# Kernel optimization log

Measured on AMD Instinct MI355X. Metric: run time of the kernel, lower is better.

The kernel has to match this reference:

```python
import jax, jax.numpy as jnp
import numpy as np

VOCAB, EMB, HID, OUT = 10, 32, 64, 10
B, T = 4096, 128

def setup_inputs() -> dict:
    key = jax.random.key(0)
    ks = jax.random.split(key, 8)
    num1 = jax.random.randint(ks[0], (B, T), 0, VOCAB, dtype=jnp.int32)
    num2 = jax.random.randint(ks[1], (B, T), 0, VOCAB, dtype=jnp.int32)
    # Glorot-ish scaled params (values irrelevant for correctness baseline)
    E = jax.random.normal(ks[2], (VOCAB, EMB), jnp.float32) * 0.05
    Wxh = jax.random.normal(ks[3], (2 * EMB, HID), jnp.float32) * (1.0 / np.sqrt(2 * EMB))
    Whh = jax.random.normal(ks[4], (HID, HID), jnp.float32) * (1.0 / np.sqrt(HID))
    b = jax.random.normal(ks[5], (HID,), jnp.float32) * 0.01
    Wd = jax.random.normal(ks[6], (HID, OUT), jnp.float32) * (1.0 / np.sqrt(HID))
    bd = jax.random.normal(ks[7], (OUT,), jnp.float32) * 0.01
    return {"num1": num1, "num2": num2, "E": E, "Wxh": Wxh, "Whh": Whh,
            "b": b, "Wd": Wd, "bd": bd}

def reference(num1, num2, E, Wxh, Whh, b, Wd, bd):
    # Embedding lookup + concat: [B, T, 2*EMB]
    x = jnp.concatenate([E[num1], E[num2]], axis=-1)
    # Precompute input projection for all timesteps (batched GEMM)
    xp = jnp.einsum('bti,ih->bth', x, Wxh) + b  # [B, T, HID]
    h0 = jnp.zeros((x.shape[0], Whh.shape[0]), x.dtype)

    def step(h, xt):  # SimpleRNNCell: h' = tanh(x W_xh + b + h W_hh)
        h = jnp.tanh(xt + h @ Whh)
        return h, h

    _, hs = jax.lax.scan(step, h0, jnp.swapaxes(xp, 0, 1))  # [T, B, HID]
    rnn_out = jnp.swapaxes(hs, 0, 1)  # return_sequences=True -> [B, T, HID]
    logits = rnn_out @ Wd + bd  # [B, T, 10]
    return logits
```

## Files before the change

kernel.cpp:

```cpp
#include <hip/hip_runtime.h>


typedef _Float16 half8 __attribute__((ext_vector_type(8)));
typedef float floatx4 __attribute__((ext_vector_type(4)));

#define MFMA16(A, B, C) __builtin_amdgcn_mfma_f32_16x16x32_f16((A), (B), (C), 0, 0, 0)
#define BARRIER() asm volatile("s_waitcnt lgkmcnt(0)\n\ts_barrier" ::: "memory")

#define HI_DW   0
#define LO_DW   9216
#define LUT_DW  10368
#define NP_DW   11392
#define POOL_DW 13472
#define LO_E    (LO_DW * 2)

__global__ __launch_bounds__(256)
void rnn_mfma(const int* __restrict__ num1, const int* __restrict__ num2,
              const float* __restrict__ E, const float* __restrict__ Wxh,
              const float* __restrict__ Whh, const float* __restrict__ bias,
              const float* __restrict__ Wd, const float* __restrict__ bd,
              float* __restrict__ out)
{
    __shared__ __align__(16) int pool[POOL_DW];
    _Float16* hiF  = (_Float16*)pool;
    int*      lutI = pool + LUT_DW;
    int*      numpk = pool + NP_DW;

    const int tid  = threadIdx.x;
    const int w    = tid >> 6;
    const int lane = tid & 63;
    const int c    = lane & 15;
    const int q    = lane >> 4;
    const int g    = blockIdx.x;

    float* WhhS = (float*)pool;
    float* P1t  = (float*)(pool + 4096);
    float* P2t  = (float*)(pool + 4736);
    float* WdS  = (float*)(pool + 5376);
    for (int i = tid; i < 4096; i += 256) WhhS[i] = Whh[i];
    for (int i = tid; i < 640;  i += 256) WdS[i]  = Wd[i];
    for (int idx = tid; idx < 640; idx += 256) {
        int v = idx >> 6, jj = idx & 63;
        float s1 = bias[jj], s2 = 0.f;
        #pragma unroll
        for (int i = 0; i < 32; ++i) {
            float e = E[v * 32 + i];
            s1 = fmaf(e, Wxh[i * 64 + jj], s1);
            s2 = fmaf(e, Wxh[(32 + i) * 64 + jj], s2);
        }
        P1t[idx] = s1;
        P2t[idx] = s2;
    }
    {
        int e = tid;
        #pragma unroll
        for (int j = 0; j < 4; ++j)
            lutI[e * 4 + j] = (((e >> (2 * j)) & 1) ? 0x3C00 : 0)
                            | (((e >> (2 * j + 1)) & 1) ? 0x3C000000 : 0);
    }
    for (int it = 0; it < 8; ++it) {
        int idx = it * 256 + tid;
        int m = idx & 15, t = idx >> 4;
        int s = g * 16 + m;
        numpk[t * 16 + m] = (1 << num1[s * 128 + t]) | (1 << (num2[s * 128 + t] + 10));
    }
    for (int i = tid; i < 576; i += 256) {
        pool[15 * 576 + i]     = 0;
        pool[LO_DW + 576 + i]  = 0;
    }
    __syncthreads();

    half8 Wf[2], Pf, Wdf[2];
    #pragma unroll
    for (int kt = 0; kt < 2; ++kt)
        #pragma unroll
        for (int j = 0; j < 8; ++j) {
            int k = kt * 32 + q * 8 + j;
            Wf[kt][j]  = (_Float16)WhhS[k * 64 + w * 16 + c];
            Wdf[kt][j] = (c < 10) ? (_Float16)WdS[k * 10 + c] : (_Float16)0.f;
        }
    #pragma unroll
    for (int j = 0; j < 8; ++j) {
        int i2 = q * 8 + j;
        float pv = (i2 < 10) ? P1t[i2 * 64 + w * 16 + c]
                 : (i2 < 20) ? P2t[(i2 - 10) * 64 + w * 16 + c] : 0.f;
        Pf[j] = (_Float16)pv;
    }
    float bdv = (c < 10) ? bd[c] : 0.f;
    __syncthreads();

    const int rvE = c * 72 + q * 8;
    const int wvE = (q * 4) * 72 + w * 16 + c;
    int pvE[2];
    pvE[0] = rvE + (2 * w + 0) * 1152;
    pvE[1] = rvE + (2 * w + 1) * 1152;

    float* outP[2][4];
    #pragma unroll
    for (int u = 0; u < 2; ++u)
        #pragma unroll
        for (int r = 0; r < 4; ++r)
            outP[u][r] = out + (((g * 16 + q * 4 + r) * 128) + 2 * w + u) * 10 + c;

    const floatx4 zero4 = {0.f, 0.f, 0.f, 0.f};

    floatx4 Cxp;
    {
        int mk = numpk[c];
        int mq = (mk >> (q * 8)) & 0xFF;
        half8 Aoh = *(const half8*)&lutI[mq * 4];
        Cxp = MFMA16(Aoh, Pf, zero4);
    }

    for (int tb = 0; tb < 128; tb += 16) {
        #pragma unroll
        for (int i = 0; i < 16; ++i) {
            int mk = numpk[(tb + i + 1) * 16 + c];

            const int sp = (i + 15) & 15;
            half8 Ah0 = *(const half8*)&hiF[sp * 1152 + rvE];
            half8 Ah1 = *(const half8*)&hiF[sp * 1152 + rvE + 32];
            half8 Al0 = *(const half8*)&hiF[LO_E + ((i + 1) & 1) * 1152 + rvE];
            half8 Al1 = *(const half8*)&hiF[LO_E + ((i + 1) & 1) * 1152 + rvE + 32];

            floatx4 C1 = MFMA16(Ah0, Wf[0], Cxp);
            C1         = MFMA16(Ah1, Wf[1], C1);
            floatx4 C2 = MFMA16(Al0, Wf[0], zero4);
            C2         = MFMA16(Al1, Wf[1], C2);

            int mq = (mk >> (q * 8)) & 0xFF;
            half8 Aoh = *(const half8*)&lutI[mq * 4];
            Cxp = MFMA16(Aoh, Pf, zero4);

            #pragma unroll
            for (int r = 0; r < 4; ++r) {
                float x  = C1[r] + C2[r] * (1.f / 2048.f);
                float e2 = __builtin_amdgcn_exp2f(x * 2.885390081777927f);
                float hv = 1.f - 2.f * __builtin_amdgcn_rcpf(e2 + 1.f);
                _Float16 hh = (_Float16)hv;
                float hif = (float)hh;
                _Float16 hl = (_Float16)((hv - hif) * 2048.f);
                hiF[i * 1152 + wvE + r * 72] = hh;
                hiF[LO_E + (i & 1) * 1152 + wvE + r * 72] = hl;
            }

            if ((i == 7 && tb != 0) || i == 15) {
                const int sb = (i == 7) ? 8 : 0;
                const int od = (i == 7) ? -80 : 0;
                #pragma unroll
                for (int u = 0; u < 2; ++u) {
                    half8 p0 = *(const half8*)&hiF[pvE[u] + sb * 1152];
                    half8 p1 = *(const half8*)&hiF[pvE[u] + sb * 1152 + 32];
                    floatx4 Cp = MFMA16(p0, Wdf[0], zero4);
                    Cp         = MFMA16(p1, Wdf[1], Cp);
                    if (c < 10) {
                        #pragma unroll
                        for (int r = 0; r < 4; ++r)
                            outP[u][r][od] = Cp[r] + bdv;
                    }
                }
            }

            BARRIER();
        }
        #pragma unroll
        for (int u = 0; u < 2; ++u)
            #pragma unroll
            for (int r = 0; r < 4; ++r)
                outP[u][r] += 160;
    }

    #pragma unroll
    for (int u = 0; u < 2; ++u) {
        half8 p0 = *(const half8*)&hiF[pvE[u] + 8 * 1152];
        half8 p1 = *(const half8*)&hiF[pvE[u] + 8 * 1152 + 32];
        floatx4 Cp = MFMA16(p0, Wdf[0], zero4);
        Cp         = MFMA16(p1, Wdf[1], Cp);
        if (c < 10) {
            #pragma unroll
            for (int r = 0; r < 4; ++r)
                outP[u][r][-80] = Cp[r] + bdv;
        }
    }
}

extern "C" void kernel_launch(void* const* d_in, const int* in_sizes, int n_in,
                              void* d_out, int out_size, void* d_ws, size_t ws_size,
                              hipStream_t stream) {
    const int*   num1 = (const int*)d_in[0];
    const int*   num2 = (const int*)d_in[1];
    const float* E    = (const float*)d_in[2];
    const float* Wxh  = (const float*)d_in[3];
    const float* Whh  = (const float*)d_in[4];
    const float* b    = (const float*)d_in[5];
    const float* Wd   = (const float*)d_in[6];
    const float* bd   = (const float*)d_in[7];
    float* out = (float*)d_out;
    rnn_mfma<<<256, 256, 0, stream>>>(num1, num2, E, Wxh, Whh, b, Wd, bd, out);
}
```

Baseline: 121.8 us.

## Interleave two sequence groups per block to hide recurrence latency

Each block now runs the RNN recurrence for two independent 16-sequence groups, interleaving their MFMA, tanh and shared-memory traffic within each timestep. The grid halves to 128 blocks and shared-memory buffers are duplicated per group. The intent is to fill MFMA and LDS latency bubbles in the serial dependency chain with independent work. The cost is half as many blocks, so fewer CUs are busy, plus more LDS use and register pressure per block.

```diff
diff --git a/kernel.cpp b/kernel.cpp
--- a/kernel.cpp
+++ b/kernel.cpp
@@ -7,12 +7,11 @@
 #define MFMA16(A, B, C) __builtin_amdgcn_mfma_f32_16x16x32_f16((A), (B), (C), 0, 0, 0)
 #define BARRIER() asm volatile("s_waitcnt lgkmcnt(0)\n\ts_barrier" ::: "memory")
 
-#define HI_DW   0
+#define G_DW    12448
 #define LO_DW   9216
-#define LUT_DW  10368
-#define NP_DW   11392
-#define POOL_DW 13472
-#define LO_E    (LO_DW * 2)
+#define NP_DW   10368
+#define LUT_DW  (2 * G_DW)
+#define POOL_DW (2 * G_DW + 1024)
 
 __global__ __launch_bounds__(256)
 void rnn_mfma(const int* __restrict__ num1, const int* __restrict__ num2,
@@ -24,7 +23,6 @@
     __shared__ __align__(16) int pool[POOL_DW];
     _Float16* hiF  = (_Float16*)pool;
     int*      lutI = pool + LUT_DW;
-    int*      numpk = pool + NP_DW;
 
     const int tid  = threadIdx.x;
     const int w    = tid >> 6;
@@ -58,15 +56,20 @@
             lutI[e * 4 + j] = (((e >> (2 * j)) & 1) ? 0x3C00 : 0)
                             | (((e >> (2 * j + 1)) & 1) ? 0x3C000000 : 0);
     }
-    for (int it = 0; it < 8; ++it) {
-        int idx = it * 256 + tid;
-        int m = idx & 15, t = idx >> 4;
-        int s = g * 16 + m;
-        numpk[t * 16 + m] = (1 << num1[s * 128 + t]) | (1 << (num2[s * 128 + t] + 10));
-    }
+    #pragma unroll
+    for (int grp = 0; grp < 2; ++grp)
+        for (int it = 0; it < 8; ++it) {
+            int idx = it * 256 + tid;
+            int m = idx & 15, t = idx >> 4;
+            int s = g * 32 + grp * 16 + m;
+            pool[grp * G_DW + NP_DW + t * 16 + m] =
+                (1 << num1[s * 128 + t]) | (1 << (num2[s * 128 + t] + 10));
+        }
     for (int i = tid; i < 576; i += 256) {
-        pool[15 * 576 + i]     = 0;
-        pool[LO_DW + 576 + i]  = 0;
+        pool[0 * G_DW + 15 * 576 + i]        = 0;
+        pool[0 * G_DW + LO_DW + 576 + i]     = 0;
+        pool[1 * G_DW + 15 * 576 + i]        = 0;
+        pool[1 * G_DW + LO_DW + 576 + i]     = 0;
     }
     __syncthreads();
 
@@ -91,72 +94,117 @@
 
     const int rvE = c * 72 + q * 8;
     const int wvE = (q * 4) * 72 + w * 16 + c;
-    int pvE[2];
-    pvE[0] = rvE + (2 * w + 0) * 1152;
-    pvE[1] = rvE + (2 * w + 1) * 1152;
-
-    float* outP[2][4];
-    #pragma unroll
-    for (int u = 0; u < 2; ++u)
-        #pragma unroll
-        for (int r = 0; r < 4; ++r)
-            outP[u][r] = out + (((g * 16 + q * 4 + r) * 128) + 2 * w + u) * 10 + c;
+    const int hi0 = 0,          lo0 = 2 * LO_DW;
+    const int hi1 = 2 * G_DW,   lo1 = 2 * G_DW + 2 * LO_DW;
+    const int* np0 = pool + NP_DW;
+    const int* np1 = pool + G_DW + NP_DW;
+
+    float* outP[2][2][4];
+    #pragma unroll
+    for (int grp = 0; grp < 2; ++grp)
+        #pragma unroll
+        for (int u = 0; u < 2; ++u)
+            #pragma unroll
+            for (int r = 0; r < 4; ++r)
+                outP[grp][u][r] = out
+                    + (((g * 32 + grp * 16 + q * 4 + r) * 128) + 2 * w + u) * 10 + c;
 
     const floatx4 zero4 = {0.f, 0.f, 0.f, 0.f};
 
-    floatx4 Cxp;
+    floatx4 Cxp0, Cxp1;
     {
-        int mk = numpk[c];
-        int mq = (mk >> (q * 8)) & 0xFF;
+        int mk = np0[c]; int mq = (mk >> (q * 8)) & 0xFF;
         half8 Aoh = *(const half8*)&lutI[mq * 4];
-        Cxp = MFMA16(Aoh, Pf, zero4);
-    }
-
-    for (int tb = 0; tb < 128; tb += 16) {
-        #pragma unroll
-        for (int i = 0; i < 16; ++i) {
-            int mk = numpk[(tb + i + 1) * 16 + c];
-
-            const int sp = (i + 15) & 15;
-            half8 Ah0 = *(const half8*)&hiF[sp * 1152 + rvE];
-            half8 Ah1 = *(const half8*)&hiF[sp * 1152 + rvE + 32];
-            half8 Al0 = *(const half8*)&hiF[LO_E + ((i + 1) & 1) * 1152 + rvE];
-            half8 Al1 = *(const half8*)&hiF[LO_E + ((i + 1) & 1) * 1152 + rvE + 32];
-
-            floatx4 C1 = MFMA16(Ah0, Wf[0], Cxp);
-            C1         = MFMA16(Ah1, Wf[1], C1);
-            floatx4 C2 = MFMA16(Al0, Wf[0], zero4);
-            C2         = MFMA16(Al1, Wf[1], C2);
-
-            int mq = (mk >> (q * 8)) & 0xFF;
-            half8 Aoh = *(const half8*)&lutI[mq * 4];
-            Cxp = MFMA16(Aoh, Pf, zero4);
+        Cxp0 = MFMA16(Aoh, Pf, zero4);
+    }
+    {
+        int mk = np1[c]; int mq = (mk >> (q * 8)) & 0xFF;
+        half8 Aoh = *(const half8*)&lutI[mq * 4];
+        Cxp1 = MFMA16(Aoh, Pf, zero4);
+    }
+
+    for (int half = 0; half < 16; ++half) {
+        const int sb  = (half & 1) * 8;
+        const int npo = half * 128 + c;
+        #pragma unroll
+        for (int i = 0; i < 8; ++i) {
+            int mk0 = np0[npo + (i + 1) * 16];
+            int mk1 = np1[npo + (i + 1) * 16];
+
+            const int spw = sb + i;
+            const int spr = (i == 0) ? ((sb ^ 8) + 7) : (sb + i - 1);
+            const int lor = ((i + 1) & 1) * 1152;
+            const int low = (i & 1) * 1152;
+
+            half8 A0h0 = *(const half8*)&hiF[hi0 + spr * 1152 + rvE];
+            half8 A0h1 = *(const half8*)&hiF[hi0 + spr * 1152 + rvE + 32];
+            half8 A0l0 = *(const half8*)&hiF[lo0 + lor + rvE];
+            half8 A0l1 = *(const half8*)&hiF[lo0 + lor + rvE + 32];
+            half8 A1h0 = *(const half8*)&hiF[hi1 + spr * 1152 + rvE];
+            half8 A1h1 = *(const half8*)&hiF[hi1 + spr * 1152 + rvE + 32];
+            half8 A1l0 = *(const half8*)&hiF[lo1 + lor + rvE];
+            half8 A1l1 = *(const half8*)&hiF[lo1 + lor + rvE + 32];
+
+            floatx4 C1a = MFMA16(A0h0, Wf[0], Cxp0);
+            C1a         = MFMA16(A0h1, Wf[1], C1a);
+            floatx4 C2a = MFMA16(A0l0, Wf[0], zero4);
+            C2a         = MFMA16(A0l1, Wf[1], C2a);
+            floatx4 C1b = MFMA16(A1h0, Wf[0], Cxp1);
+            C1b         = MFMA16(A1h1, Wf[1], C1b);
+            floatx4 C2b = MFMA16(A1l0, Wf[0], zero4);
+            C2b         = MFMA16(A1l1, Wf[1], C2b);
+
+            {
+                int mq = (mk0 >> (q * 8)) & 0xFF;
+                half8 Aoh = *(const half8*)&lutI[mq * 4];
+                Cxp0 = MFMA16(Aoh, Pf, zero4);
+            }
+            {
+                int mq = (mk1 >> (q * 8)) & 0xFF;
+                half8 Aoh = *(const half8*)&lutI[mq * 4];
+                Cxp1 = MFMA16(Aoh, Pf, zero4);
+            }
 
             #pragma unroll
             for (int r = 0; r < 4; ++r) {
-                float x  = C1[r] + C2[r] * (1.f / 2048.f);
+                float x  = C1a[r] + C2a[r] * (1.f / 2048.f);
                 float e2 = __builtin_amdgcn_exp2f(x * 2.885390081777927f);
                 float hv = 1.f - 2.f * __builtin_amdgcn_rcpf(e2 + 1.f);
                 _Float16 hh = (_Float16)hv;
                 float hif = (float)hh;
                 _Float16 hl = (_Float16)((hv - hif) * 2048.f);
-                hiF[i * 1152 + wvE + r * 72] = hh;
-                hiF[LO_E + (i & 1) * 1152 + wvE + r * 72] = hl;
-            }
-
-            if ((i == 7 && tb != 0) || i == 15) {
-                const int sb = (i == 7) ? 8 : 0;
-                const int od = (i == 7) ? -80 : 0;
+                hiF[hi0 + spw * 1152 + wvE + r * 72] = hh;
+                hiF[lo0 + low + wvE + r * 72] = hl;
+            }
+            #pragma unroll
+            for (int r = 0; r < 4; ++r) {
+                float x  = C1b[r] + C2b[r] * (1.f / 2048.f);
+                float e2 = __builtin_amdgcn_exp2f(x * 2.885390081777927f);
+                float hv = 1.f - 2.f * __builtin_amdgcn_rcpf(e2 + 1.f);
+                _Float16 hh = (_Float16)hv;
+                float hif = (float)hh;
+                _Float16 hl = (_Float16)((hv - hif) * 2048.f);
+                hiF[hi1 + spw * 1152 + wvE + r * 72] = hh;
+                hiF[lo1 + low + wvE + r * 72] = hl;
+            }
+
+            if (i == 7 && half > 0) {
+                const int sbp = (half & 1) ? 0 : 8;
                 #pragma unroll
-                for (int u = 0; u < 2; ++u) {
-                    half8 p0 = *(const half8*)&hiF[pvE[u] + sb * 1152];
-                    half8 p1 = *(const half8*)&hiF[pvE[u] + sb * 1152 + 32];
-                    floatx4 Cp = MFMA16(p0, Wdf[0], zero4);
-                    Cp         = MFMA16(p1, Wdf[1], Cp);
-                    if (c < 10) {
-                        #pragma unroll
-                        for (int r = 0; r < 4; ++r)
-                            outP[u][r][od] = Cp[r] + bdv;
+                for (int grp = 0; grp < 2; ++grp) {
+                    const int gh = grp ? hi1 : hi0;
+                    #pragma unroll
+                    for (int u = 0; u < 2; ++u) {
+                        const int pv = gh + (sbp + 2 * w + u) * 1152 + rvE;
+                        half8 p0 = *(const half8*)&hiF[pv];
+                        half8 p1 = *(const half8*)&hiF[pv + 32];
+                        floatx4 Cp = MFMA16(p0, Wdf[0], zero4);
+                        Cp         = MFMA16(p1, Wdf[1], Cp);
+                        if (c < 10) {
+                            #pragma unroll
+                            for (int r = 0; r < 4; ++r)
+                                outP[grp][u][r][-80] = Cp[r] + bdv;
+                        }
                     }
                 }
             }
@@ -164,22 +212,29 @@
             BARRIER();
         }
         #pragma unroll
-        for (int u = 0; u < 2; ++u)
-            #pragma unroll
-            for (int r = 0; r < 4; ++r)
-                outP[u][r] += 160;
-    }
-
-    #pragma unroll
-    for (int u = 0; u < 2; ++u) {
-        half8 p0 = *(const half8*)&hiF[pvE[u] + 8 * 1152];
-        half8 p1 = *(const half8*)&hiF[pvE[u] + 8 * 1152 + 32];
-        floatx4 Cp = MFMA16(p0, Wdf[0], zero4);
-        Cp         = MFMA16(p1, Wdf[1], Cp);
-        if (c < 10) {
-            #pragma unroll
-            for (int r = 0; r < 4; ++r)
-                outP[u][r][-80] = Cp[r] + bdv;
+        for (int grp = 0; grp < 2; ++grp)
+            #pragma unroll
+            for (int u = 0; u < 2; ++u)
+                #pragma unroll
+                for (int r = 0; r < 4; ++r)
+                    outP[grp][u][r] += 80;
+    }
+
+    #pragma unroll
+    for (int grp = 0; grp < 2; ++grp) {
+        const int gh = grp ? hi1 : hi0;
+        #pragma unroll
+        for (int u = 0; u < 2; ++u) {
+            const int pv = gh + (8 + 2 * w + u) * 1152 + rvE;
+            half8 p0 = *(const half8*)&hiF[pv];
+            half8 p1 = *(const half8*)&hiF[pv + 32];
+            floatx4 Cp = MFMA16(p0, Wdf[0], zero4);
+            Cp         = MFMA16(p1, Wdf[1], Cp);
+            if (c < 10) {
+                #pragma unroll
+                for (int r = 0; r < 4; ++r)
+                    outP[grp][u][r][-80] = Cp[r] + bdv;
+            }
         }
     }
 }
@@ -196,5 +251,5 @@
     const float* Wd   = (const float*)d_in[6];
     const float* bd   = (const float*)d_in[7];
     float* out = (float*)d_out;
-    rnn_mfma<<<256, 256, 0, stream>>>(num1, num2, E, Wxh, Whh, b, Wd, bd, out);
+    rnn_mfma<<<128, 256, 0, stream>>>(num1, num2, E, Wxh, Whh, b, Wd, bd, out);
 }
```

Result: slower. 158.4 us (+30.0%).

## Pack two 16-sequence recurrence groups into each 512-thread block

Applied to the files above, without the earlier changes.

Each block now runs two independent groups of 16 sequences with 8 waves, and the grid is halved to 128 blocks. Each group has its own hidden-state ring buffers and token masks in shared memory, while the weight LUT and setup are shared. The step loop is restructured into 8-step halves that write outputs for the previous half. The intent is to interleave two independent recurrence chains per CU, hiding MFMA and LDS latency and amortising setup. The cost is that half the CUs sit idle, LDS use roughly doubles, and both groups are coupled by a shared barrier every step.

```diff
diff --git a/kernel.cpp b/kernel.cpp
--- a/kernel.cpp
+++ b/kernel.cpp
@@ -7,14 +7,13 @@
 #define MFMA16(A, B, C) __builtin_amdgcn_mfma_f32_16x16x32_f16((A), (B), (C), 0, 0, 0)
 #define BARRIER() asm volatile("s_waitcnt lgkmcnt(0)\n\ts_barrier" ::: "memory")
 
-#define HI_DW   0
+#define G_DW    12448
 #define LO_DW   9216
-#define LUT_DW  10368
-#define NP_DW   11392
-#define POOL_DW 13472
-#define LO_E    (LO_DW * 2)
-
-__global__ __launch_bounds__(256)
+#define NP_DW   10368
+#define LUT_DW  (2 * G_DW)
+#define POOL_DW (2 * G_DW + 1024)
+
+__global__ __launch_bounds__(512)
 void rnn_mfma(const int* __restrict__ num1, const int* __restrict__ num2,
               const float* __restrict__ E, const float* __restrict__ Wxh,
               const float* __restrict__ Whh, const float* __restrict__ bias,
@@ -24,10 +23,11 @@
     __shared__ __align__(16) int pool[POOL_DW];
     _Float16* hiF  = (_Float16*)pool;
     int*      lutI = pool + LUT_DW;
-    int*      numpk = pool + NP_DW;
 
     const int tid  = threadIdx.x;
-    const int w    = tid >> 6;
+    const int w8   = tid >> 6;
+    const int grp  = w8 >> 2;
+    const int w    = w8 & 3;
     const int lane = tid & 63;
     const int c    = lane & 15;
     const int q    = lane >> 4;
@@ -37,9 +37,9 @@
     float* P1t  = (float*)(pool + 4096);
     float* P2t  = (float*)(pool + 4736);
     float* WdS  = (float*)(pool + 5376);
-    for (int i = tid; i < 4096; i += 256) WhhS[i] = Whh[i];
-    for (int i = tid; i < 640;  i += 256) WdS[i]  = Wd[i];
-    for (int idx = tid; idx < 640; idx += 256) {
+    for (int i = tid; i < 4096; i += 512) WhhS[i] = Whh[i];
+    for (int i = tid; i < 640;  i += 512) WdS[i]  = Wd[i];
+    for (int idx = tid; idx < 640; idx += 512) {
         int v = idx >> 6, jj = idx & 63;
         float s1 = bias[jj], s2 = 0.f;
         #pragma unroll
@@ -51,22 +51,25 @@
         P1t[idx] = s1;
         P2t[idx] = s2;
     }
-    {
+    if (tid < 256) {
         int e = tid;
         #pragma unroll
         for (int j = 0; j < 4; ++j)
             lutI[e * 4 + j] = (((e >> (2 * j)) & 1) ? 0x3C00 : 0)
                             | (((e >> (2 * j + 1)) & 1) ? 0x3C000000 : 0);
     }
-    for (int it = 0; it < 8; ++it) {
-        int idx = it * 256 + tid;
-        int m = idx & 15, t = idx >> 4;
-        int s = g * 16 + m;
-        numpk[t * 16 + m] = (1 << num1[s * 128 + t]) | (1 << (num2[s * 128 + t] + 10));
-    }
-    for (int i = tid; i < 576; i += 256) {
-        pool[15 * 576 + i]     = 0;
-        pool[LO_DW + 576 + i]  = 0;
+    for (int idx = tid; idx < 4096; idx += 512) {
+        int gp = idx >> 11;
+        int m = idx & 15, t = (idx >> 4) & 127;
+        int s = g * 32 + gp * 16 + m;
+        pool[gp * G_DW + NP_DW + t * 16 + m] =
+            (1 << num1[s * 128 + t]) | (1 << (num2[s * 128 + t] + 10));
+    }
+    for (int i = tid; i < 576; i += 512) {
+        pool[0 * G_DW + 15 * 576 + i]    = 0;
+        pool[0 * G_DW + LO_DW + 576 + i] = 0;
+        pool[1 * G_DW + 15 * 576 + i]    = 0;
+        pool[1 * G_DW + LO_DW + 576 + i] = 0;
     }
     __syncthreads();
 
@@ -91,46 +94,55 @@
 
     const int rvE = c * 72 + q * 8;
     const int wvE = (q * 4) * 72 + w * 16 + c;
-    int pvE[2];
-    pvE[0] = rvE + (2 * w + 0) * 1152;
-    pvE[1] = rvE + (2 * w + 1) * 1152;
+    const int hiE = grp * (2 * G_DW);
+    const int loE = hiE + 2 * LO_DW;
+    const int* np = pool + grp * G_DW + NP_DW;
 
     float* outP[2][4];
     #pragma unroll
     for (int u = 0; u < 2; ++u)
         #pragma unroll
         for (int r = 0; r < 4; ++r)
-            outP[u][r] = out + (((g * 16 + q * 4 + r) * 128) + 2 * w + u) * 10 + c;
+            outP[u][r] = out
+                + (((g * 32 + grp * 16 + q * 4 + r) * 128) + 2 * w + u) * 10 + c;
 
     const floatx4 zero4 = {0.f, 0.f, 0.f, 0.f};
 
     floatx4 Cxp;
     {
-        int mk = numpk[c];
+        int mk = np[c];
         int mq = (mk >> (q * 8)) & 0xFF;
         half8 Aoh = *(const half8*)&lutI[mq * 4];
         Cxp = MFMA16(Aoh, Pf, zero4);
     }
 
-    for (int tb = 0; tb < 128; tb += 16) {
-        #pragma unroll
-        for (int i = 0; i < 16; ++i) {
-            int mk = numpk[(tb + i + 1) * 16 + c];
-
-            const int sp = (i + 15) & 15;
-            half8 Ah0 = *(const half8*)&hiF[sp * 1152 + rvE];
-            half8 Ah1 = *(const half8*)&hiF[sp * 1152 + rvE + 32];
-            half8 Al0 = *(const half8*)&hiF[LO_E + ((i + 1) & 1) * 1152 + rvE];
-            half8 Al1 = *(const half8*)&hiF[LO_E + ((i + 1) & 1) * 1152 + rvE + 32];
+    for (int half = 0; half < 16; ++half) {
+        const int sb  = (half & 1) * 8;
+        const int npo = half * 128 + c;
+        #pragma unroll
+        for (int i = 0; i < 8; ++i) {
+            int mk = np[npo + (i + 1) * 16];
+
+            const int spw = sb + i;
+            const int spr = (i == 0) ? ((sb ^ 8) + 7) : (sb + i - 1);
+            const int lor = ((i + 1) & 1) * 1152;
+            const int low = (i & 1) * 1152;
+
+            half8 Ah0 = *(const half8*)&hiF[hiE + spr * 1152 + rvE];
+            half8 Ah1 = *(const half8*)&hiF[hiE + spr * 1152 + rvE + 32];
+            half8 Al0 = *(const half8*)&hiF[loE + lor + rvE];
+            half8 Al1 = *(const half8*)&hiF[loE + lor + rvE + 32];
 
             floatx4 C1 = MFMA16(Ah0, Wf[0], Cxp);
             C1         = MFMA16(Ah1, Wf[1], C1);
             floatx4 C2 = MFMA16(Al0, Wf[0], zero4);
             C2         = MFMA16(Al1, Wf[1], C2);
 
-            int mq = (mk >> (q * 8)) & 0xFF;
-            half8 Aoh = *(const half8*)&lutI[mq * 4];
-            Cxp = MFMA16(Aoh, Pf, zero4);
+            {
+                int mq = (mk >> (q * 8)) & 0xFF;
+                half8 Aoh = *(const half8*)&lutI[mq * 4];
+                Cxp = MFMA16(Aoh, Pf, zero4);
+            }
 
             #pragma unroll
             for (int r = 0; r < 4; ++r) {
@@ -140,23 +152,23 @@
                 _Float16 hh = (_Float16)hv;
                 float hif = (float)hh;
                 _Float16 hl = (_Float16)((hv - hif) * 2048.f);
-                hiF[i * 1152 + wvE + r * 72] = hh;
-                hiF[LO_E + (i & 1) * 1152 + wvE + r * 72] = hl;
+                hiF[hiE + spw * 1152 + wvE + r * 72] = hh;
+                hiF[loE + low + wvE + r * 72] = hl;
             }
 
-            if ((i == 7 && tb != 0) || i == 15) {
-                const int sb = (i == 7) ? 8 : 0;
-                const int od = (i == 7) ? -80 : 0;
+            if (i == 7 && half > 0) {
+                const int sbp = (half & 1) ? 0 : 8;
                 #pragma unroll
                 for (int u = 0; u < 2; ++u) {
-                    half8 p0 = *(const half8*)&hiF[pvE[u] + sb * 1152];
-                    half8 p1 = *(const half8*)&hiF[pvE[u] + sb * 1152 + 32];
+                    const int pv = hiE + (sbp + 2 * w + u) * 1152 + rvE;
+                    half8 p0 = *(const half8*)&hiF[pv];
+                    half8 p1 = *(const half8*)&hiF[pv + 32];
                     floatx4 Cp = MFMA16(p0, Wdf[0], zero4);
                     Cp         = MFMA16(p1, Wdf[1], Cp);
                     if (c < 10) {
                         #pragma unroll
                         for (int r = 0; r < 4; ++r)
-                            outP[u][r][od] = Cp[r] + bdv;
+                            outP[u][r][-80] = Cp[r] + bdv;
                     }
                 }
             }
@@ -167,13 +179,14 @@
         for (int u = 0; u < 2; ++u)
             #pragma unroll
             for (int r = 0; r < 4; ++r)
-                outP[u][r] += 160;
+                outP[u][r] += 80;
     }
 
     #pragma unroll
     for (int u = 0; u < 2; ++u) {
-        half8 p0 = *(const half8*)&hiF[pvE[u] + 8 * 1152];
-        half8 p1 = *(const half8*)&hiF[pvE[u] + 8 * 1152 + 32];
+        const int pv = hiE + (8 + 2 * w + u) * 1152 + rvE;
+        half8 p0 = *(const half8*)&hiF[pv];
+        half8 p1 = *(const half8*)&hiF[pv + 32];
         floatx4 Cp = MFMA16(p0, Wdf[0], zero4);
         Cp         = MFMA16(p1, Wdf[1], Cp);
         if (c < 10) {
@@ -196,5 +209,5 @@
     const float* Wd   = (const float*)d_in[6];
     const float* bd   = (const float*)d_in[7];
     float* out = (float*)d_out;
-    rnn_mfma<<<256, 256, 0, stream>>>(num1, num2, E, Wxh, Whh, b, Wd, bd, out);
+    rnn_mfma<<<128, 512, 0, stream>>>(num1, num2, E, Wxh, Whh, b, Wd, bd, out);
 }
```

New measurement: 139.5 us. 14.5% more time.

## Interleave hi/lo fp16 hidden-state split into a single MFMA operand layout

Applied to the files above, without the earlier changes.

The hidden state is now stored as interleaved hi/lo fp16 pairs in one shared buffer, with the lo part scaled by 64. Whh and Wd are expanded into matching interleaved [w, w/64] fragments, so each step reads four contiguous half8 vectors instead of separate hi and lo buffers, and the two partial sums add directly. Packing uses cvt_pkrtz and perm, and the output projection is rescheduled to run at steps 2 and 6 of every 8-step half-block. The goal is simpler LDS addressing and cheaper hi/lo conversion. The cost is more LDS, plus round-toward-zero conversion and a coarser lo scale that change numerics.

```diff
diff --git a/kernel.cpp b/kernel.cpp
--- a/kernel.cpp
+++ b/kernel.cpp
@@ -2,17 +2,15 @@
 
 
 typedef _Float16 half8 __attribute__((ext_vector_type(8)));
+typedef __fp16 fp16x2 __attribute__((ext_vector_type(2)));
 typedef float floatx4 __attribute__((ext_vector_type(4)));
 
 #define MFMA16(A, B, C) __builtin_amdgcn_mfma_f32_16x16x32_f16((A), (B), (C), 0, 0, 0)
 #define BARRIER() asm volatile("s_waitcnt lgkmcnt(0)\n\ts_barrier" ::: "memory")
 
-#define HI_DW   0
-#define LO_DW   9216
-#define LUT_DW  10368
-#define NP_DW   11392
-#define POOL_DW 13472
-#define LO_E    (LO_DW * 2)
+#define LUT_DW  17408
+#define NP_DW   18432
+#define POOL_DW 20512
 
 __global__ __launch_bounds__(256)
 void rnn_mfma(const int* __restrict__ num1, const int* __restrict__ num2,
@@ -22,9 +20,8 @@
               float* __restrict__ out)
 {
     __shared__ __align__(16) int pool[POOL_DW];
-    _Float16* hiF  = (_Float16*)pool;
-    int*      lutI = pool + LUT_DW;
-    int*      numpk = pool + NP_DW;
+    int* lutI  = pool + LUT_DW;
+    int* numpk = pool + NP_DW;
 
     const int tid  = threadIdx.x;
     const int w    = tid >> 6;
@@ -58,26 +55,26 @@
             lutI[e * 4 + j] = (((e >> (2 * j)) & 1) ? 0x3C00 : 0)
                             | (((e >> (2 * j + 1)) & 1) ? 0x3C000000 : 0);
     }
-    for (int it = 0; it < 8; ++it) {
-        int idx = it * 256 + tid;
+    for (int idx = tid; idx < 2080; idx += 256) {
         int m = idx & 15, t = idx >> 4;
         int s = g * 16 + m;
-        numpk[t * 16 + m] = (1 << num1[s * 128 + t]) | (1 << (num2[s * 128 + t] + 10));
-    }
-    for (int i = tid; i < 576; i += 256) {
-        pool[15 * 576 + i]     = 0;
-        pool[LO_DW + 576 + i]  = 0;
+        numpk[t * 16 + m] = (t < 128)
+            ? ((1 << num1[s * 128 + t]) | (1 << (num2[s * 128 + t] + 10))) : 0;
     }
     __syncthreads();
 
-    half8 Wf[2], Pf, Wdf[2];
-    #pragma unroll
-    for (int kt = 0; kt < 2; ++kt)
-        #pragma unroll
-        for (int j = 0; j < 8; ++j) {
-            int k = kt * 32 + q * 8 + j;
-            Wf[kt][j]  = (_Float16)WhhS[k * 64 + w * 16 + c];
-            Wdf[kt][j] = (c < 10) ? (_Float16)WdS[k * 10 + c] : (_Float16)0.f;
+    half8 Wint[4], Wdint[4], Pf;
+    #pragma unroll
+    for (int kt = 0; kt < 4; ++kt)
+        #pragma unroll
+        for (int p = 0; p < 4; ++p) {
+            int k = kt * 16 + q * 4 + p;
+            float wv = WhhS[k * 64 + w * 16 + c];
+            Wint[kt][2 * p]     = (_Float16)wv;
+            Wint[kt][2 * p + 1] = (_Float16)(wv * 0.015625f);
+            float dv = (c < 10) ? WdS[k * 10 + c] : 0.f;
+            Wdint[kt][2 * p]     = (_Float16)dv;
+            Wdint[kt][2 * p + 1] = (_Float16)(dv * 0.015625f);
         }
     #pragma unroll
     for (int j = 0; j < 8; ++j) {
@@ -89,11 +86,11 @@
     float bdv = (c < 10) ? bd[c] : 0.f;
     __syncthreads();
 
-    const int rvE = c * 72 + q * 8;
-    const int wvE = (q * 4) * 72 + w * 16 + c;
-    int pvE[2];
-    pvE[0] = rvE + (2 * w + 0) * 1152;
-    pvE[1] = rvE + (2 * w + 1) * 1152;
+    for (int i = tid; i < 1088; i += 256) pool[15 * 1088 + i] = 0;
+    __syncthreads();
+
+    const int rBase = c * 68 + q * 4;
+    const int wBase = (q * 4) * 68 + w * 16 + c;
 
     float* outP[2][4];
     #pragma unroll
@@ -112,52 +109,70 @@
         Cxp = MFMA16(Aoh, Pf, zero4);
     }
 
-    for (int tb = 0; tb < 128; tb += 16) {
-        #pragma unroll
-        for (int i = 0; i < 16; ++i) {
-            int mk = numpk[(tb + i + 1) * 16 + c];
-
-            const int sp = (i + 15) & 15;
-            half8 Ah0 = *(const half8*)&hiF[sp * 1152 + rvE];
-            half8 Ah1 = *(const half8*)&hiF[sp * 1152 + rvE + 32];
-            half8 Al0 = *(const half8*)&hiF[LO_E + ((i + 1) & 1) * 1152 + rvE];
-            half8 Al1 = *(const half8*)&hiF[LO_E + ((i + 1) & 1) * 1152 + rvE + 32];
-
-            floatx4 C1 = MFMA16(Ah0, Wf[0], Cxp);
-            C1         = MFMA16(Ah1, Wf[1], C1);
-            floatx4 C2 = MFMA16(Al0, Wf[0], zero4);
-            C2         = MFMA16(Al1, Wf[1], C2);
-
-            int mq = (mk >> (q * 8)) & 0xFF;
-            half8 Aoh = *(const half8*)&lutI[mq * 4];
-            Cxp = MFMA16(Aoh, Pf, zero4);
-
+    for (int half = 0; half < 16; ++half) {
+        const int sb  = (half & 1) * 8;
+        const int npo = half * 128 + c;
+        #pragma unroll
+        for (int i = 0; i < 8; ++i) {
+            int mk = numpk[npo + (i + 1) * 16];
+
+            const int spw = sb + i;
+            const int spr = (i == 0) ? ((sb ^ 8) + 7) : (sb + i - 1);
+
+            half8 A0 = *(const half8*)&pool[spr * 1088 + rBase];
+            half8 A1 = *(const half8*)&pool[spr * 1088 + rBase + 16];
+            half8 A2 = *(const half8*)&pool[spr * 1088 + rBase + 32];
+            half8 A3 = *(const half8*)&pool[spr * 1088 + rBase + 48];
+
+            floatx4 Ca = MFMA16(A0, Wint[0], Cxp);
+            Ca         = MFMA16(A1, Wint[1], Ca);
+            floatx4 Cb = MFMA16(A2, Wint[2], zero4);
+            Cb         = MFMA16(A3, Wint[3], Cb);
+
+            {
+                int mq = (mk >> (q * 8)) & 0xFF;
+                half8 Aoh = *(const half8*)&lutI[mq * 4];
+                Cxp = MFMA16(Aoh, Pf, zero4);
+            }
+
+            float hv[4];
             #pragma unroll
             for (int r = 0; r < 4; ++r) {
-                float x  = C1[r] + C2[r] * (1.f / 2048.f);
+                float x  = Ca[r] + Cb[r];
                 float e2 = __builtin_amdgcn_exp2f(x * 2.885390081777927f);
-                float hv = 1.f - 2.f * __builtin_amdgcn_rcpf(e2 + 1.f);
-                _Float16 hh = (_Float16)hv;
-                float hif = (float)hh;
-                _Float16 hl = (_Float16)((hv - hif) * 2048.f);
-                hiF[i * 1152 + wvE + r * 72] = hh;
-                hiF[LO_E + (i & 1) * 1152 + wvE + r * 72] = hl;
-            }
-
-            if ((i == 7 && tb != 0) || i == 15) {
-                const int sb = (i == 7) ? 8 : 0;
-                const int od = (i == 7) ? -80 : 0;
-                #pragma unroll
-                for (int u = 0; u < 2; ++u) {
-                    half8 p0 = *(const half8*)&hiF[pvE[u] + sb * 1152];
-                    half8 p1 = *(const half8*)&hiF[pvE[u] + sb * 1152 + 32];
-                    floatx4 Cp = MFMA16(p0, Wdf[0], zero4);
-                    Cp         = MFMA16(p1, Wdf[1], Cp);
-                    if (c < 10) {
-                        #pragma unroll
-                        for (int r = 0; r < 4; ++r)
-                            outP[u][r][od] = Cp[r] + bdv;
-                    }
+                hv[r] = 1.f - 2.f * __builtin_amdgcn_rcpf(e2 + 1.f);
+            }
+            #pragma unroll
+            for (int p = 0; p < 2; ++p) {
+                fp16x2 ph = __builtin_amdgcn_cvt_pkrtz(hv[2 * p], hv[2 * p + 1]);
+                float c0 = (float)ph[0];
+                float c1 = (float)ph[1];
+                fp16x2 pl = __builtin_amdgcn_cvt_pkrtz((hv[2 * p] - c0) * 64.f,
+                                                       (hv[2 * p + 1] - c1) * 64.f);
+                unsigned phu = __builtin_bit_cast(unsigned, ph);
+                unsigned plu = __builtin_bit_cast(unsigned, pl);
+                unsigned w0 = __builtin_amdgcn_perm(plu, phu, 0x05040100u);
+                unsigned w1 = __builtin_amdgcn_perm(plu, phu, 0x07060302u);
+                pool[spw * 1088 + wBase + (2 * p) * 68]     = (int)w0;
+                pool[spw * 1088 + wBase + (2 * p + 1) * 68] = (int)w1;
+            }
+
+            if ((i == 2 || i == 6) && half > 0) {
+                const int u   = (i == 6);
+                const int sbp = (half & 1) ? 0 : 8;
+                const int sl  = (sbp + 2 * w + u) * 1088 + rBase;
+                half8 P0 = *(const half8*)&pool[sl];
+                half8 P1 = *(const half8*)&pool[sl + 16];
+                half8 P2 = *(const half8*)&pool[sl + 32];
+                half8 P3 = *(const half8*)&pool[sl + 48];
+                floatx4 Cp = MFMA16(P0, Wdint[0], zero4);
+                Cp         = MFMA16(P1, Wdint[1], Cp);
+                Cp         = MFMA16(P2, Wdint[2], Cp);
+                Cp         = MFMA16(P3, Wdint[3], Cp);
+                if (c < 10) {
+                    #pragma unroll
+                    for (int r = 0; r < 4; ++r)
+                        outP[u][r][-80] = Cp[r] + bdv;
                 }
             }
 
@@ -167,15 +182,20 @@
         for (int u = 0; u < 2; ++u)
             #pragma unroll
             for (int r = 0; r < 4; ++r)
-                outP[u][r] += 160;
+                outP[u][r] += 80;
     }
 
     #pragma unroll
     for (int u = 0; u < 2; ++u) {
-        half8 p0 = *(const half8*)&hiF[pvE[u] + 8 * 1152];
-        half8 p1 = *(const half8*)&hiF[pvE[u] + 8 * 1152 + 32];
-        floatx4 Cp = MFMA16(p0, Wdf[0], zero4);
-        Cp         = MFMA16(p1, Wdf[1], Cp);
+        const int sl = (8 + 2 * w + u) * 1088 + rBase;
+        half8 P0 = *(const half8*)&pool[sl];
+        half8 P1 = *(const half8*)&pool[sl + 16];
+        half8 P2 = *(const half8*)&pool[sl + 32];
+        half8 P3 = *(const half8*)&pool[sl + 48];
+        floatx4 Cp = MFMA16(P0, Wdint[0], zero4);
+        Cp         = MFMA16(P1, Wdint[1], Cp);
+        Cp         = MFMA16(P2, Wdint[2], Cp);
+        Cp         = MFMA16(P3, Wdint[3], Cp);
         if (c < 10) {
             #pragma unroll
             for (int r = 0; r < 4; ++r)
```

Result: no change. 119.8 us (-1.6%).
